# Kernel tuning notes

Measured on AMD Instinct MI355X. Metric: run time of the kernel, lower is better.

The kernel has to match this reference:

```python
import jax, jax.numpy as jnp
import numpy as np
import math

N = 12288
IN_MAIN, IN_MOD = 64, 128
NC_INNER, NC_QK, OUT_MAIN = 16, 8, 64

def setup_inputs() -> dict:
    key = jax.random.key(0)
    ks = jax.random.split(key, 8)
    s = lambda fan_in: 1.0 / np.sqrt(fan_in)
    return {
        "x_main": jax.random.normal(ks[0], (N, IN_MAIN), dtype=jnp.float32),
        "x_mod": jax.random.normal(ks[1], (N, IN_MOD), dtype=jnp.float32),
        "xyz": jax.random.uniform(ks[2], (N, 3), dtype=jnp.float32),
        # MLP E: [in_main+in_mod -> nc_inner -> nc_inner], bias=False (weights stored [in, out])
        "W_e1": jax.random.uniform(ks[3], (IN_MAIN + IN_MOD, NC_INNER), jnp.float32, -s(IN_MAIN + IN_MOD), s(IN_MAIN + IN_MOD)),
        "W_e2": jax.random.uniform(ks[4], (NC_INNER, NC_INNER), jnp.float32, -s(NC_INNER), s(NC_INNER)),
        "W_q": jax.random.uniform(ks[5], (NC_INNER, NC_QK), jnp.float32, -s(NC_INNER), s(NC_INNER)),
        "W_k": jax.random.uniform(ks[6], (NC_INNER, NC_QK), jnp.float32, -s(NC_INNER), s(NC_INNER)),
        "W_v": jax.random.uniform(ks[7], (NC_INNER, OUT_MAIN), jnp.float32, -s(NC_INNER), s(NC_INNER)),
    }

def reference(x_main, x_mod, xyz, W_e1, W_e2, W_q, W_k, W_v):
    # concat 3D + 2D features: [N, in_main+in_mod]
    x = jnp.concatenate((x_main, x_mod), axis=-1)
    # MLP E (bias-free Linear + ReLU per layer): [N, nc_inner]
    h = jax.nn.relu(jax.nn.relu(x @ W_e1) @ W_e2)
    Q = h @ W_q  # [N, nc_qk]
    K = h @ W_k  # [N, nc_qk]
    V = h @ W_v  # [N, out_main]
    scale = 1.0 / math.sqrt(NC_QK)
    scores = (Q @ K.T) * scale          # [N, N] full global attention
    attn = jax.nn.softmax(scores, axis=1)
    return attn @ V                     # [N, out_main]
```

## Files before the change

### kernel.cpp

```cpp
#include <hip/hip_runtime.h>
#include <stdint.h>


#define NN 12288

typedef float    f32x16 __attribute__((ext_vector_type(16)));
typedef short    s16x8  __attribute__((ext_vector_type(8)));
typedef unsigned short u16;

#define MFMA_32x32x16_BF16 __builtin_amdgcn_mfma_f32_32x32x16_bf16

#define OFF_QB   0u
#define OFF_KB   196608u
#define OFF_VT   393216u
#define OFF_PO   2162688u

typedef __attribute__((address_space(3))) void lds_void_t;
typedef const __attribute__((address_space(1))) void gbl_void_t;
__device__ __forceinline__ void gld16(const void* g, void* l) {
    __builtin_amdgcn_global_load_lds((gbl_void_t*)g, (lds_void_t*)l, 16, 0, 0);
}

__device__ __forceinline__ float bf2f(u16 s) {
    union { unsigned int u; float f; } c; c.u = ((unsigned int)s) << 16; return c.f;
}
__device__ __forceinline__ u16 f2bf(float f) {
    union { float f; unsigned int u; } c; c.f = f;
    return (u16)((c.u + 0x8000u) >> 16);
}
__device__ __forceinline__ unsigned int pk2(float a, float b) {
    union { float f; unsigned int u; } ca, cb; ca.f = a; cb.f = b;
    return ((ca.u + 0x8000u) >> 16) | ((cb.u + 0x8000u) & 0xffff0000u);
}
__device__ __forceinline__ unsigned int pkbf(float a, float b) {
#if __has_builtin(__builtin_amdgcn_cvt_pk_bf16_f32)
    auto r = __builtin_amdgcn_cvt_pk_bf16_f32(a, b);
    union { decltype(r) v; unsigned int u; } c; c.v = r; return c.u;
#else
    return pk2(a, b);
#endif
}
__device__ __forceinline__ f32x16 zf16() {
    f32x16 z;
#pragma unroll
    for (int i = 0; i < 16; ++i) z[i] = 0.f;
    return z;
}
__device__ __forceinline__ s16x8 zs8() {
    s16x8 z;
#pragma unroll
    for (int i = 0; i < 8; ++i) z[i] = 0;
    return z;
}

union U8 { s16x8 v; unsigned int u[4]; };

__global__ __launch_bounds__(256) void k1_qkv(
    const void* __restrict__ xmain, const void* __restrict__ xmod,
    const void* __restrict__ we1, const void* __restrict__ we2,
    const void* __restrict__ wqp, const void* __restrict__ wkp,
    const void* __restrict__ wvp,
    u16* __restrict__ qb, u16* __restrict__ kb, u16* __restrict__ vt)
{
    __shared__ float wf[4608];
    __shared__ int   sflag;
    __shared__ float lh1[64][4][17];
    __shared__ float lh2[64][17];

    const int t = threadIdx.x;
    const int r = t >> 2;
    const int p = t & 3;
    const int row = blockIdx.x * 64 + r;

    if (t == 0) sflag = 0;
    __syncthreads();
    {
        float v = bf2f(((const u16*)xmod)[2 * t]);
        if (fabsf(v) > 16.f) atomicAdd(&sflag, 1);
    }
    __syncthreads();
    const int isf32 = (sflag > 8);

    const float SCL = 0.51006979f;
    if (isf32) {
        const float* a1 = (const float*)we1; const float* a2 = (const float*)we2;
        const float* aq = (const float*)wqp; const float* ak = (const float*)wkp;
        const float* av = (const float*)wvp;
        for (int i = t; i < 4608; i += 256) {
            if      (i < 3072) wf[i] = a1[i];
            else if (i < 3328) wf[i] = a2[i - 3072];
            else if (i < 3456) wf[i] = aq[i - 3328] * SCL;
            else if (i < 3584) wf[i] = ak[i - 3456];
            else               wf[i] = av[i - 3584];
        }
    } else {
        const u16* a1 = (const u16*)we1; const u16* a2 = (const u16*)we2;
        const u16* aq = (const u16*)wqp; const u16* ak = (const u16*)wkp;
        const u16* av = (const u16*)wvp;
        for (int i = t; i < 4608; i += 256) {
            if      (i < 3072) wf[i] = bf2f(a1[i]);
            else if (i < 3328) wf[i] = bf2f(a2[i - 3072]);
            else if (i < 3456) wf[i] = bf2f(aq[i - 3328]) * SCL;
            else if (i < 3584) wf[i] = bf2f(ak[i - 3456]);
            else               wf[i] = bf2f(av[i - 3584]);
        }
    }
    __syncthreads();

    const float* __restrict__ W1 = wf;
    const float* __restrict__ W2 = wf + 3072;
    const float* __restrict__ Wq = wf + 3328;
    const float* __restrict__ Wk = wf + 3456;
    const float* __restrict__ Wv = wf + 3584;

    float h1p[16];
#pragma unroll
    for (int o = 0; o < 16; ++o) h1p[o] = 0.f;

    if (isf32) {
#pragma unroll
        for (int cc = 0; cc < 12; ++cc) {
            const int c = p + cc * 4;
            float4 xv = (c < 16)
                ? ((const float4*)xmain)[(size_t)row * 16 + c]
                : ((const float4*)xmod)[(size_t)row * 32 + (c - 16)];
            float xs[4] = {xv.x, xv.y, xv.z, xv.w};
#pragma unroll
            for (int j = 0; j < 4; ++j) {
                const float* wr = W1 + (c * 4 + j) * 16;
#pragma unroll
                for (int o = 0; o < 16; ++o) h1p[o] += xs[j] * wr[o];
            }
        }
    } else {
#pragma unroll
        for (int cc = 0; cc < 12; ++cc) {
            const int c = p + cc * 4;
            uint2 xv = (c < 16)
                ? ((const uint2*)xmain)[(size_t)row * 16 + c]
                : ((const uint2*)xmod)[(size_t)row * 32 + (c - 16)];
            float xs[4] = { bf2f((u16)(xv.x & 0xffff)), bf2f((u16)(xv.x >> 16)),
                            bf2f((u16)(xv.y & 0xffff)), bf2f((u16)(xv.y >> 16)) };
#pragma unroll
            for (int j = 0; j < 4; ++j) {
                const float* wr = W1 + (c * 4 + j) * 16;
#pragma unroll
                for (int o = 0; o < 16; ++o) h1p[o] += xs[j] * wr[o];
            }
        }
    }
#pragma unroll
    for (int o = 0; o < 16; ++o) lh1[r][p][o] = h1p[o];
    __syncthreads();

    float h1[16];
#pragma unroll
    for (int o = 0; o < 16; ++o)
        h1[o] = fmaxf(lh1[r][0][o] + lh1[r][1][o] + lh1[r][2][o] + lh1[r][3][o], 0.f);

#pragma unroll
    for (int oo = 0; oo < 4; ++oo) {
        const int o = p * 4 + oo;
        float s = 0.f;
#pragma unroll
        for (int j = 0; j < 16; ++j) s += h1[j] * W2[j * 16 + o];
        lh2[r][o] = fmaxf(s, 0.f);
    }
    __syncthreads();

    float h2[16];
#pragma unroll
    for (int j = 0; j < 16; ++j) h2[j] = lh2[r][j];

    {
        float q0 = 0.f, q1 = 0.f, k0 = 0.f, k1 = 0.f;
        const int o = 2 * p;
#pragma unroll
        for (int j = 0; j < 16; ++j) {
            q0 += h2[j] * Wq[j * 8 + o];
            q1 += h2[j] * Wq[j * 8 + o + 1];
            k0 += h2[j] * Wk[j * 8 + o];
            k1 += h2[j] * Wk[j * 8 + o + 1];
        }
        ((unsigned int*)qb)[(size_t)row * 4 + p] = pk2(q0, q1);
        ((unsigned int*)kb)[(size_t)row * 4 + p] = pk2(k0, k1);
    }

    const int tI = row >> 5, kk = row & 31;
#pragma unroll
    for (int c16 = 0; c16 < 16; ++c16) {
        const int c = p * 16 + c16;
        float v = 0.f;
#pragma unroll
        for (int j = 0; j < 16; ++j) v += h2[j] * Wv[j * 64 + c];
        vt[(size_t)tI * 2304 + c * 36 + kk] = f2bf(v);
    }
}

__global__ __launch_bounds__(256, 6) void k2_attn(
    const u16* __restrict__ qb, const u16* __restrict__ kb,
    const u16* __restrict__ vt,
    u16* __restrict__ po, float* __restrict__ pl,
    int nsplit, int tiles)
{
    __shared__ union SM {
        uint4 stage[2][288];
        float sf[2304];
    } sm;

    const int tid  = threadIdx.x;
    const int lane = tid & 63;
    const int half = lane >> 5;
    const int l31  = lane & 31;
    const int w    = tid >> 6;
    const int qB   = (blockIdx.x % 96) * 128;
    const int sp   = blockIdx.x / 96;
    const int myq  = qB + 32 * w;
    const int key_start = sp * (NN / nsplit);
    const int t0 = key_start >> 5;

    const f32x16 Z = zf16();
    s16x8 qf = zs8();
    if (!half) qf = *(const s16x8*)(qb + (size_t)(myq + l31) * 8);

    f32x16 acc0 = Z, acc1 = Z;
    float ls = 0.f;

    {
        const char* g = (const char*)vt + (size_t)t0 * 4608 + 1152 * w + lane * 16;
        char* l = (char*)&sm.stage[0][0] + 1152 * w;
        gld16(g, l);
        if (lane < 8) gld16(g + 1024, l + 1024);
    }
    s16x8 ka_c = *(const s16x8*)(kb + (size_t)(key_start + l31) * 8);

    for (int kt = 0; kt < tiles; ++kt) {
        __builtin_amdgcn_s_waitcnt(0x0F70);
        __syncthreads();
        const int cb = kt & 1;
        const bool has_next = (kt + 1 < tiles);

        s16x8 ka_n;
        if (has_next) {
            ka_n = *(const s16x8*)(kb + (size_t)(key_start + (kt + 1) * 32 + l31) * 8);
            const char* g = (const char*)vt + (size_t)(t0 + kt + 1) * 4608
                          + 1152 * w + lane * 16;
            char* l = (char*)&sm.stage[cb ^ 1][0] + 1152 * w;
            gld16(g, l);
            if (lane < 8) gld16(g + 1024, l + 1024);
        }

        f32x16 S = MFMA_32x32x16_BF16(ka_c, qf, Z, 0, 0, 0);

        float pr[16];
        float ls0 = 0.f, ls1 = 0.f;
#pragma unroll
        for (int r = 0; r < 8; ++r) {
            pr[r]     = __builtin_amdgcn_exp2f(S[r]);
            pr[r + 8] = __builtin_amdgcn_exp2f(S[r + 8]);
            ls0 += pr[r];
            ls1 += pr[r + 8];
        }
        ls += ls0 + ls1;

        U8 pb0, pb1;
#pragma unroll
        for (int i = 0; i < 4; ++i) {
            pb0.u[i] = pkbf(pr[2 * i],     pr[2 * i + 1]);
            pb1.u[i] = pkbf(pr[8 + 2 * i], pr[8 + 2 * i + 1]);
        }

        const u16* base = (const u16*)&sm.stage[cb][0];
        const u16* r0 = base + l31 * 36 + 4 * half;
        const u16* r1 = base + (32 + l31) * 36 + 4 * half;
        U8 va;
        uint2 x0, x1;
        x0 = *(const uint2*)(r0);       x1 = *(const uint2*)(r0 + 8);
        va.u[0] = x0.x; va.u[1] = x0.y; va.u[2] = x1.x; va.u[3] = x1.y;
        acc0 = MFMA_32x32x16_BF16(va.v, pb0.v, acc0, 0, 0, 0);
        x0 = *(const uint2*)(r1);       x1 = *(const uint2*)(r1 + 8);
        va.u[0] = x0.x; va.u[1] = x0.y; va.u[2] = x1.x; va.u[3] = x1.y;
        acc1 = MFMA_32x32x16_BF16(va.v, pb0.v, acc1, 0, 0, 0);
        x0 = *(const uint2*)(r0 + 16);  x1 = *(const uint2*)(r0 + 24);
        va.u[0] = x0.x; va.u[1] = x0.y; va.u[2] = x1.x; va.u[3] = x1.y;
        acc0 = MFMA_32x32x16_BF16(va.v, pb1.v, acc0, 0, 0, 0);
        x0 = *(const uint2*)(r1 + 16);  x1 = *(const uint2*)(r1 + 24);
        va.u[0] = x0.x; va.u[1] = x0.y; va.u[2] = x1.x; va.u[3] = x1.y;
        acc1 = MFMA_32x32x16_BF16(va.v, pb1.v, acc1, 0, 0, 0);

        if (has_next) ka_c = ka_n;
    }

    ls += __shfl_xor(ls, 32, 64);

    u16* poS = po + (size_t)sp * (NN * 64);
    for (int j = 0; j < 4; ++j) {
        __syncthreads();
        if (w == j) {
#pragma unroll
            for (int r = 0; r < 16; ++r) {
                const int c = (r & 3) + 8 * (r >> 2) + 4 * half;
                sm.sf[c * 33 + l31]        = acc0[r];
                sm.sf[(32 + c) * 33 + l31] = acc1[r];
            }
            if (lane < 32) sm.sf[2112 + l31] = ls;
        }
        __syncthreads();
        const int rq = tid >> 3;
        const int c0 = (tid & 7) * 8;
        unsigned int u0 = pkbf(sm.sf[(c0 + 0) * 33 + rq], sm.sf[(c0 + 1) * 33 + rq]);
        unsigned int u1 = pkbf(sm.sf[(c0 + 2) * 33 + rq], sm.sf[(c0 + 3) * 33 + rq]);
        unsigned int u2 = pkbf(sm.sf[(c0 + 4) * 33 + rq], sm.sf[(c0 + 5) * 33 + rq]);
        unsigned int u3 = pkbf(sm.sf[(c0 + 6) * 33 + rq], sm.sf[(c0 + 7) * 33 + rq]);
        *(uint4*)(poS + (size_t)(qB + 32 * j + rq) * 64 + c0) =
            make_uint4(u0, u1, u2, u3);
        if (tid < 32)
            pl[(size_t)sp * NN + qB + 32 * j + tid] = sm.sf[2112 + tid];
    }
}

__global__ __launch_bounds__(256) void k3_norm(
    const u16* __restrict__ po, const float* __restrict__ pl,
    float4* __restrict__ out, int nsplit)
{
    const int i = blockIdx.x * 256 + threadIdx.x;
    const int row = i >> 4;
    const int c0 = (i & 15) * 4;
    float l = 0.f;
    float o0 = 0.f, o1 = 0.f, o2 = 0.f, o3 = 0.f;
    for (int s = 0; s < nsplit; ++s) {
        l += pl[(size_t)s * NN + row];
        uint2 p = *(const uint2*)(po + (size_t)s * (NN * 64) +
                                  (size_t)row * 64 + c0);
        o0 += bf2f((u16)(p.x & 0xffff)); o1 += bf2f((u16)(p.x >> 16));
        o2 += bf2f((u16)(p.y & 0xffff)); o3 += bf2f((u16)(p.y >> 16));
    }
    const float rl = 1.0f / l;
    out[i] = make_float4(o0 * rl, o1 * rl, o2 * rl, o3 * rl);
}

extern "C" void kernel_launch(void* const* d_in, const int* in_sizes, int n_in,
                              void* d_out, int out_size, void* d_ws, size_t ws_size,
                              hipStream_t stream)
{
    const void* xmain = d_in[0];
    const void* xmod  = d_in[1];
    const void* we1   = d_in[3];
    const void* we2   = d_in[4];
    const void* wq    = d_in[5];
    const void* wk    = d_in[6];
    const void* wv    = d_in[7];

    char* ws = (char*)d_ws;
    u16*   qb   = (u16*)  (ws + OFF_QB);
    u16*   kb   = (u16*)  (ws + OFF_KB);
    u16*   vt   = (u16*)  (ws + OFF_VT);

    int S = 1;
    for (int cand = 16; cand >= 1; cand >>= 1) {
        size_t need = (size_t)OFF_PO + (size_t)cand * (NN * 64 * 2) +
                      (size_t)cand * (NN * 4);
        if (ws_size >= need) { S = cand; break; }
    }
    u16*   po = (u16*)(ws + OFF_PO);
    float* pl = (float*)(ws + OFF_PO + (size_t)S * (NN * 64 * 2));
    const int tiles = NN / (32 * S);

    k1_qkv<<<192, 256, 0, stream>>>(xmain, xmod, we1, we2, wq, wk, wv,
                                    qb, kb, vt);
    k2_attn<<<96 * S, 256, 0, stream>>>(qb, kb, vt, po, pl, S, tiles);
    k3_norm<<<768, 256, 0, stream>>>(po, pl, (float4*)d_out, S);
}
```

Baseline: 132.6 us.

## Process two key tiles per iteration and compute softmax row sums via MFMA

The attention loop now handles 64 keys per iteration with a doubled LDS staging buffer, which halves the number of barriers and waitcnt stalls per key. The scalar per-lane exp summation and the final cross-half shuffle are replaced by an extra MFMA against a ones vector that accumulates the row sums on the matrix unit. The sums now come from bf16-rounded probabilities, which changes numerics slightly. The extra MFMAs, extra accumulator registers and larger LDS use may reduce occupancy below the launch-bounds target.

```diff
diff --git a/kernel.cpp b/kernel.cpp
--- a/kernel.cpp
+++ b/kernel.cpp
@@ -197,14 +197,51 @@
     }
 }
 
+
+__device__ __forceinline__ void tile_pv(
+    const f32x16& S, const u16* __restrict__ base, int l31, int half,
+    const s16x8& ones, f32x16& acc0, f32x16& acc1, f32x16& accl)
+{
+    float pr[16];
+#pragma unroll
+    for (int r = 0; r < 16; ++r) pr[r] = __builtin_amdgcn_exp2f(S[r]);
+
+    U8 p0, p1;
+#pragma unroll
+    for (int i = 0; i < 4; ++i) {
+        p0.u[i] = pkbf(pr[2 * i],     pr[2 * i + 1]);
+        p1.u[i] = pkbf(pr[8 + 2 * i], pr[8 + 2 * i + 1]);
+    }
+
+    accl = MFMA_32x32x16_BF16(ones, p0.v, accl, 0, 0, 0);
+    accl = MFMA_32x32x16_BF16(ones, p1.v, accl, 0, 0, 0);
+
+    const u16* r0 = base + l31 * 36 + 4 * half;
+    const u16* r1 = base + (32 + l31) * 36 + 4 * half;
+    U8 va;
+    uint2 x0, x1;
+    x0 = *(const uint2*)(r0);       x1 = *(const uint2*)(r0 + 8);
+    va.u[0] = x0.x; va.u[1] = x0.y; va.u[2] = x1.x; va.u[3] = x1.y;
+    acc0 = MFMA_32x32x16_BF16(va.v, p0.v, acc0, 0, 0, 0);
+    x0 = *(const uint2*)(r1);       x1 = *(const uint2*)(r1 + 8);
+    va.u[0] = x0.x; va.u[1] = x0.y; va.u[2] = x1.x; va.u[3] = x1.y;
+    acc1 = MFMA_32x32x16_BF16(va.v, p0.v, acc1, 0, 0, 0);
+    x0 = *(const uint2*)(r0 + 16);  x1 = *(const uint2*)(r0 + 24);
+    va.u[0] = x0.x; va.u[1] = x0.y; va.u[2] = x1.x; va.u[3] = x1.y;
+    acc0 = MFMA_32x32x16_BF16(va.v, p1.v, acc0, 0, 0, 0);
+    x0 = *(const uint2*)(r1 + 16);  x1 = *(const uint2*)(r1 + 24);
+    va.u[0] = x0.x; va.u[1] = x0.y; va.u[2] = x1.x; va.u[3] = x1.y;
+    acc1 = MFMA_32x32x16_BF16(va.v, p1.v, acc1, 0, 0, 0);
+}
+
 __global__ __launch_bounds__(256, 6) void k2_attn(
     const u16* __restrict__ qb, const u16* __restrict__ kb,
     const u16* __restrict__ vt,
     u16* __restrict__ po, float* __restrict__ pl,
-    int nsplit, int tiles)
+    int nsplit, int niter)
 {
     __shared__ union SM {
-        uint4 stage[2][288];
+        uint4 stage[2][576];
         float sf[2304];
     } sm;
 
@@ -217,81 +254,59 @@
     const int sp   = blockIdx.x / 96;
     const int myq  = qB + 32 * w;
     const int key_start = sp * (NN / nsplit);
-    const int t0 = key_start >> 5;
+    const int c0 = key_start >> 6;
 
     const f32x16 Z = zf16();
     s16x8 qf = zs8();
     if (!half) qf = *(const s16x8*)(qb + (size_t)(myq + l31) * 8);
 
-    f32x16 acc0 = Z, acc1 = Z;
-    float ls = 0.f;
+    s16x8 ones;
+#pragma unroll
+    for (int i = 0; i < 8; ++i) ones[i] = (short)0x3F80;
+
+    f32x16 acc0 = Z, acc1 = Z, accl = Z;
 
     {
-        const char* g = (const char*)vt + (size_t)t0 * 4608 + 1152 * w + lane * 16;
-        char* l = (char*)&sm.stage[0][0] + 1152 * w;
+        const char* g = (const char*)vt + (size_t)c0 * 9216 + 2304 * w + lane * 16;
+        char* l = (char*)&sm.stage[0][0] + 2304 * w;
         gld16(g, l);
-        if (lane < 8) gld16(g + 1024, l + 1024);
-    }
-    s16x8 ka_c = *(const s16x8*)(kb + (size_t)(key_start + l31) * 8);
-
-    for (int kt = 0; kt < tiles; ++kt) {
+        gld16(g + 1024, l + 1024);
+        if (lane < 16) gld16(g + 2048, l + 2048);
+    }
+    const s16x8* kp = (const s16x8*)kb;
+    s16x8 ka_c0 = kp[key_start + l31];
+    s16x8 ka_c1 = kp[key_start + 32 + l31];
+
+    for (int it = 0; it < niter; ++it) {
         __builtin_amdgcn_s_waitcnt(0x0F70);
         __syncthreads();
-        const int cb = kt & 1;
-        const bool has_next = (kt + 1 < tiles);
-
-        s16x8 ka_n;
+        const int cb = it & 1;
+        const bool has_next = (it + 1 < niter);
+
+        s16x8 ka_n0, ka_n1;
         if (has_next) {
-            ka_n = *(const s16x8*)(kb + (size_t)(key_start + (kt + 1) * 32 + l31) * 8);
-            const char* g = (const char*)vt + (size_t)(t0 + kt + 1) * 4608
-                          + 1152 * w + lane * 16;
-            char* l = (char*)&sm.stage[cb ^ 1][0] + 1152 * w;
+            const int nk = key_start + (it + 1) * 64 + l31;
+            ka_n0 = kp[nk];
+            ka_n1 = kp[nk + 32];
+            const char* g = (const char*)vt + (size_t)(c0 + it + 1) * 9216
+                          + 2304 * w + lane * 16;
+            char* l = (char*)&sm.stage[cb ^ 1][0] + 2304 * w;
             gld16(g, l);
-            if (lane < 8) gld16(g + 1024, l + 1024);
-        }
-
-        f32x16 S = MFMA_32x32x16_BF16(ka_c, qf, Z, 0, 0, 0);
-
-        float pr[16];
-        float ls0 = 0.f, ls1 = 0.f;
-#pragma unroll
-        for (int r = 0; r < 8; ++r) {
-            pr[r]     = __builtin_amdgcn_exp2f(S[r]);
-            pr[r + 8] = __builtin_amdgcn_exp2f(S[r + 8]);
-            ls0 += pr[r];
-            ls1 += pr[r + 8];
-        }
-        ls += ls0 + ls1;
-
-        U8 pb0, pb1;
-#pragma unroll
-        for (int i = 0; i < 4; ++i) {
-            pb0.u[i] = pkbf(pr[2 * i],     pr[2 * i + 1]);
-            pb1.u[i] = pkbf(pr[8 + 2 * i], pr[8 + 2 * i + 1]);
-        }
-
-        const u16* base = (const u16*)&sm.stage[cb][0];
-        const u16* r0 = base + l31 * 36 + 4 * half;
-        const u16* r1 = base + (32 + l31) * 36 + 4 * half;
-        U8 va;
-        uint2 x0, x1;
-        x0 = *(const uint2*)(r0);       x1 = *(const uint2*)(r0 + 8);
-        va.u[0] = x0.x; va.u[1] = x0.y; va.u[2] = x1.x; va.u[3] = x1.y;
-        acc0 = MFMA_32x32x16_BF16(va.v, pb0.v, acc0, 0, 0, 0);
-        x0 = *(const uint2*)(r1);       x1 = *(const uint2*)(r1 + 8);
-        va.u[0] = x0.x; va.u[1] = x0.y; va.u[2] = x1.x; va.u[3] = x1.y;
-        acc1 = MFMA_32x32x16_BF16(va.v, pb0.v, acc1, 0, 0, 0);
-        x0 = *(const uint2*)(r0 + 16);  x1 = *(const uint2*)(r0 + 24);
-        va.u[0] = x0.x; va.u[1] = x0.y; va.u[2] = x1.x; va.u[3] = x1.y;
-        acc0 = MFMA_32x32x16_BF16(va.v, pb1.v, acc0, 0, 0, 0);
-        x0 = *(const uint2*)(r1 + 16);  x1 = *(const uint2*)(r1 + 24);
-        va.u[0] = x0.x; va.u[1] = x0.y; va.u[2] = x1.x; va.u[3] = x1.y;
-        acc1 = MFMA_32x32x16_BF16(va.v, pb1.v, acc1, 0, 0, 0);
-
-        if (has_next) ka_c = ka_n;
-    }
-
-    ls += __shfl_xor(ls, 32, 64);
+            gld16(g + 1024, l + 1024);
+            if (lane < 16) gld16(g + 2048, l + 2048);
+        }
+
+        f32x16 Sa = MFMA_32x32x16_BF16(ka_c0, qf, Z, 0, 0, 0);
+        f32x16 Sb = MFMA_32x32x16_BF16(ka_c1, qf, Z, 0, 0, 0);
+
+        const u16* baseA = (const u16*)&sm.stage[cb][0];
+        tile_pv(Sa, baseA,        l31, half, ones, acc0, acc1, accl);
+        tile_pv(Sb, baseA + 2304, l31, half, ones, acc0, acc1, accl);
+
+        if (has_next) { ka_c0 = ka_n0; ka_c1 = ka_n1; }
+    }
+
+    const float ls = accl[0];
 
     u16* poS = po + (size_t)sp * (NN * 64);
     for (int j = 0; j < 4; ++j) {
@@ -307,12 +322,12 @@
         }
         __syncthreads();
         const int rq = tid >> 3;
-        const int c0 = (tid & 7) * 8;
-        unsigned int u0 = pkbf(sm.sf[(c0 + 0) * 33 + rq], sm.sf[(c0 + 1) * 33 + rq]);
-        unsigned int u1 = pkbf(sm.sf[(c0 + 2) * 33 + rq], sm.sf[(c0 + 3) * 33 + rq]);
-        unsigned int u2 = pkbf(sm.sf[(c0 + 4) * 33 + rq], sm.sf[(c0 + 5) * 33 + rq]);
-        unsigned int u3 = pkbf(sm.sf[(c0 + 6) * 33 + rq], sm.sf[(c0 + 7) * 33 + rq]);
-        *(uint4*)(poS + (size_t)(qB + 32 * j + rq) * 64 + c0) =
+        const int c0b = (tid & 7) * 8;
+        unsigned int u0 = pkbf(sm.sf[(c0b + 0) * 33 + rq], sm.sf[(c0b + 1) * 33 + rq]);
+        unsigned int u1 = pkbf(sm.sf[(c0b + 2) * 33 + rq], sm.sf[(c0b + 3) * 33 + rq]);
+        unsigned int u2 = pkbf(sm.sf[(c0b + 4) * 33 + rq], sm.sf[(c0b + 5) * 33 + rq]);
+        unsigned int u3 = pkbf(sm.sf[(c0b + 6) * 33 + rq], sm.sf[(c0b + 7) * 33 + rq]);
+        *(uint4*)(poS + (size_t)(qB + 32 * j + rq) * 64 + c0b) =
             make_uint4(u0, u1, u2, u3);
         if (tid < 32)
             pl[(size_t)sp * NN + qB + 32 * j + tid] = sm.sf[2112 + tid];
@@ -364,10 +379,10 @@
     }
     u16*   po = (u16*)(ws + OFF_PO);
     float* pl = (float*)(ws + OFF_PO + (size_t)S * (NN * 64 * 2));
-    const int tiles = NN / (32 * S);
+    const int niter = NN / (64 * S);
 
     k1_qkv<<<192, 256, 0, stream>>>(xmain, xmod, we1, we2, wq, wk, wv,
                                     qb, kb, vt);
-    k2_attn<<<96 * S, 256, 0, stream>>>(qb, kb, vt, po, pl, S, tiles);
+    k2_attn<<<96 * S, 256, 0, stream>>>(qb, kb, vt, po, pl, S, niter);
     k3_norm<<<768, 256, 0, stream>>>(po, pl, (float4*)d_out, S);
 }
```

After: 186.6 us. 1.41x slower.
